# Optimization experiments

Hardware: AMD Instinct MI355X
Metric: run time of the kernel (lower is better)

Reference implementation:

```python
import jax, jax.numpy as jnp
import numpy as np

EPS = 1e-5

def setup_inputs() -> dict:
    key = jax.random.key(0)
    k1, k2, k3 = jax.random.split(key, 3)
    B, D, T = 16, 512, 1024
    K = 8192
    x = jax.random.normal(k1, (B, D, T), dtype=jnp.float32)
    embedding_sum = jax.random.normal(k2, (K, D), dtype=jnp.float32)
    cluster_usage = jax.random.uniform(k3, (K,), dtype=jnp.float32)
    return {"x": x, "embedding_sum": embedding_sum, "cluster_usage": cluster_usage}

def reference(x, embedding_sum, cluster_usage):
    # embedding = embedding_sum / clamp(cluster_usage, eps)  -> [K, D]
    emb = embedding_sum / jnp.clip(cluster_usage, EPS, None)[:, None]
    B, D, T = x.shape
    # encode: [B, D, T] -> [B*T, D]
    xf = jnp.transpose(x, (0, 2, 1)).reshape(B * T, D)
    # squared Euclidean distance (argmin-equivalent to cdist p=2)
    x2 = jnp.sum(xf * xf, axis=1, keepdims=True)          # [N, 1]
    e2 = jnp.sum(emb * emb, axis=1)                        # [K]
    d2 = x2 - 2.0 * (xf @ emb.T) + e2[None, :]             # [N, K]
    codes = jnp.argmin(d2, axis=-1).reshape(B, 1, T)       # [B, 1, T]
    # decode: gather codebook vectors
    quantized = emb[codes[:, 0, :]]                        # [B, T, D]
    quantized = jnp.transpose(quantized, (0, 2, 1))        # [B, D, T]
    return codes, quantized
```

## Files before the change

kernel.cpp:

```cpp
#include <hip/hip_runtime.h>
#include <hip/hip_bf16.h>
#include <cfloat>
#include <stdint.h>

#define EPS 1e-5f
constexpr int Dd = 512, Tt = 1024, Kk = 8192;
constexpr int Nq = 16 * 1024;
constexpr float TAU = 1.5f;

typedef __bf16 bf16x8 __attribute__((ext_vector_type(8)));
typedef float  f32x4  __attribute__((ext_vector_type(4)));
typedef unsigned long long u64;

union Pack8 { __bf16 h[8]; int4 v; };

__device__ __forceinline__ void gld16(const void* g, void* l) {
    __builtin_amdgcn_global_load_lds(
        (const __attribute__((address_space(1))) uint32_t*)g,
        (__attribute__((address_space(3))) uint32_t*)l, 16, 0, 0);
}

__device__ __forceinline__ unsigned monokey(float s) {
    unsigned b = __float_as_uint(s);
    return b ^ ((unsigned)((int)b >> 31) | 0x80000000u);
}
__device__ __forceinline__ float unmono(unsigned u) {
    u = (u & 0x80000000u) ? (u ^ 0x80000000u) : ~u;
    return __uint_as_float(u);
}

__device__ __forceinline__ void merge2u(unsigned& a1, unsigned& a2, unsigned b1, unsigned b2) {
    unsigned c1 = min(a1, b1);
    unsigned c2 = min(max(a1, b1), min(a2, b2));
    a1 = c1; a2 = c2;
}
__device__ __forceinline__ u64 umin64(u64 a, u64 b) { return a < b ? a : b; }
__device__ __forceinline__ u64 umax64(u64 a, u64 b) { return a > b ? a : b; }
__device__ __forceinline__ void merge4q(u64& a1, u64& a2, u64& a3, u64& a4,
                                        u64 b1, u64 b2, u64 b3, u64 b4) {
    u64 c1 = umin64(a1, b1);
    u64 c2 = umin64(umin64(a2, b2), umax64(a1, b1));
    u64 c3 = umin64(umin64(a3, b3), umin64(umax64(a2, b1), umax64(a1, b2)));
    u64 c4 = umin64(umin64(a4, b4), umin64(umax64(a3, b1), umax64(a1, b3)));
    c4 = umin64(c4, umax64(a2, b2));
    a1 = c1; a2 = c2; a3 = c3; a4 = c4;
}
__device__ __forceinline__ u64 shflx64(u64 v, int m) {
    int lo = __shfl_xor((int)(unsigned)v, m, 64);
    int hi = __shfl_xor((int)(v >> 32), m, 64);
    return ((u64)(unsigned)hi << 32) | (unsigned)lo;
}

__global__ __launch_bounds__(256) void split_x_kernel(const float* __restrict__ x,
                                                      ushort* __restrict__ Xh,
                                                      float* __restrict__ Xf,
                                                      int* __restrict__ cnt) {
    if (blockIdx.x == 0 && threadIdx.x < 2) cnt[threadIdx.x] = 0;
    __shared__ float Ls[64][68];
    const int tid = threadIdx.x, bid = blockIdx.x;
    const int b  = bid >> 7;
    const int d0 = ((bid >> 4) & 7) * 64;
    const int t0 = (bid & 15) * 64;
    const float* xb = x + ((size_t)b * Dd + d0) * Tt + t0;
#pragma unroll
    for (int it = 0; it < 4; ++it) {
        int s = it * 256 + tid;
        int d = s >> 4, c = (s & 15) * 4;
        float4 g = *(const float4*)(xb + (size_t)d * Tt + c);
        *(float4*)&Ls[d][c] = g;
    }
    __syncthreads();
    const int t = tid >> 2;
    const int dseg = (tid & 3) * 16;
    Pack8 ph[2];
    float vf[16];
#pragma unroll
    for (int dd = 0; dd < 16; ++dd) {
        float v = Ls[dseg + dd][t];
        vf[dd] = v;
        ph[dd >> 3].h[dd & 7] = (__bf16)v;
    }
    size_t base = ((size_t)(b * Tt + t0 + t)) * Dd + d0 + dseg;
    *(int4*)(Xh + base)     = ph[0].v;
    *(int4*)(Xh + base + 8) = ph[1].v;
#pragma unroll
    for (int g = 0; g < 4; ++g)
        *(float4*)(Xf + base + g * 4) = make_float4(vf[g*4], vf[g*4+1], vf[g*4+2], vf[g*4+3]);
}

__global__ __launch_bounds__(256) void split_e_kernel(const float* __restrict__ es,
                                                      const float* __restrict__ usage,
                                                      ushort* __restrict__ Eh,
                                                      float* __restrict__ embf,
                                                      double* __restrict__ e2d,
                                                      float* __restrict__ e2f) {
    const int wave = threadIdx.x >> 6, lane = threadIdx.x & 63;
    const int k = blockIdx.x * 4 + wave;
    const float uc = fmaxf(usage[k], EPS);
    const float* row = es + (size_t)k * Dd;
    const int d = lane * 8;
    float4 a = *(const float4*)(row + d);
    float4 c = *(const float4*)(row + d + 4);
    float ef[8] = {a.x/uc, a.y/uc, a.z/uc, a.w/uc, c.x/uc, c.y/uc, c.z/uc, c.w/uc};
    Pack8 ph;
    double e2 = 0.0;
#pragma unroll
    for (int j = 0; j < 8; ++j) {
        ph.h[j] = (__bf16)ef[j];
        e2 = fma((double)ef[j], (double)ef[j], e2);
    }
    size_t base = (size_t)k * Dd + d;
    *(int4*)(Eh + base) = ph.v;
    *(float4*)(embf + base)     = make_float4(ef[0], ef[1], ef[2], ef[3]);
    *(float4*)(embf + base + 4) = make_float4(ef[4], ef[5], ef[6], ef[7]);
#pragma unroll
    for (int off = 32; off >= 1; off >>= 1) e2 += __shfl_down(e2, off, 64);
    if (lane == 0) { e2d[k] = e2; e2f[k] = (float)e2; }
}

__device__ __forceinline__ void stageA2(const ushort* __restrict__ Xh, char* buf,
                                        int m0, int d0, int tid, int j0) {
#pragma unroll
    for (int j = 0; j < 2; ++j) {
        int s = (j0 + j) * 512 + tid;
        int row = s >> 3;
        int clog = (s & 7) ^ (row & 7);
        gld16(Xh + (size_t)(m0 + row) * Dd + d0 + clog * 8, buf + s * 16);
    }
}
__device__ __forceinline__ void stageB2(const ushort* __restrict__ Eh, char* buf,
                                        int n0, int d0, int tid, int j0) {
#pragma unroll
    for (int j = 0; j < 2; ++j) {
        int s = (j0 + j) * 512 + tid;
        int row = s >> 3;
        int clog = (s & 7) ^ (row & 7);
        gld16(Eh + (size_t)(n0 + row) * Dd + d0 + clog * 8, buf + 32768 + s * 16);
    }
}

#define SB() __builtin_amdgcn_sched_barrier(0)

__global__ __launch_bounds__(512) void gemm_kernel(const ushort* __restrict__ Xh,
                                                   const ushort* __restrict__ Eh,
                                                   const float* __restrict__ e2f,
                                                   uint2* __restrict__ colres) {
    __shared__ int4 ldsbuf[8192];
    char* lds = (char*)ldsbuf;

    const int tid = threadIdx.x;
    int wg = blockIdx.x;
    int wgid = (wg & 7) * 256 + (wg >> 3);
    int st = wgid >> 5, u = wgid & 31;
    int mb = (st >> 3) * 8 + (u & 7);
    int nb = (st & 7) * 4 + (u >> 3);
    const int m0 = mb * 256, n0 = nb * 256;

    const int wave = tid >> 6, lane = tid & 63;
    const int wm = wave >> 1, wn = wave & 1;
    const int mw = wm * 64, nw = wn * 128;
    const int fm = lane & 15, fq = lane >> 4;
    const int fm7 = fm & 7;
    const int x0 = (fq ^ fm7) * 16;
    const int x1 = ((4 + fq) ^ fm7) * 16;

    f32x4 acc[8][4] = {};

    stageA2(Xh, lds, m0, 0, tid, 0);
    stageA2(Xh, lds, m0, 0, tid, 2);
    stageB2(Eh, lds, n0, 0, tid, 0);
    stageB2(Eh, lds, n0, 0, tid, 2);
    stageA2(Xh, lds + 65536, m0, 64, tid, 0);
    asm volatile("s_waitcnt vmcnt(2)" ::: "memory");
    __builtin_amdgcn_s_barrier();
    SB();

    for (int t = 0; t < 8; ++t) {
        char* bufc = lds + (t & 1) * 65536;
        char* bufn = lds + ((t + 1) & 1) * 65536;
        const char* pA = bufc + (mw + fm) * 128;
        const char* pB = bufc + 32768 + (nw + fm) * 128;
        const int d1 = (t + 1) * 64, d2 = (t + 2) * 64;
        bf16x8 a0[4], a1[4], fr[4];

#pragma unroll
        for (int i = 0; i < 4; ++i) a0[i] = *(const bf16x8*)(pA + i * 2048 + x0);
#pragma unroll
        for (int i = 0; i < 4; ++i) fr[i] = *(const bf16x8*)(pB + i * 2048 + x0);
        SB();
        if (t + 1 < 8) stageA2(Xh, bufn, m0, d1, tid, 2);
        SB();
        __builtin_amdgcn_s_barrier();
        asm volatile("s_waitcnt lgkmcnt(0)" ::: "memory");
        SB();
        __builtin_amdgcn_s_setprio(1);
#pragma unroll
        for (int i = 0; i < 4; ++i)
#pragma unroll
            for (int j = 0; j < 4; ++j)
                acc[i][j] = __builtin_amdgcn_mfma_f32_16x16x32_bf16(fr[i], a0[j], acc[i][j], 0, 0, 0);
        __builtin_amdgcn_s_setprio(0);
        SB();
        __builtin_amdgcn_s_barrier();

#pragma unroll
        for (int i = 0; i < 4; ++i) fr[i] = *(const bf16x8*)(pB + 8192 + i * 2048 + x0);
        SB();
        if (t + 1 < 8) stageB2(Eh, bufn, n0, d1, tid, 0);
        SB();
        __builtin_amdgcn_s_barrier();
        asm volatile("s_waitcnt lgkmcnt(0)" ::: "memory");
        SB();
        __builtin_amdgcn_s_setprio(1);
#pragma unroll
        for (int i = 0; i < 4; ++i)
#pragma unroll
            for (int j = 0; j < 4; ++j)
                acc[i + 4][j] = __builtin_amdgcn_mfma_f32_16x16x32_bf16(fr[i], a0[j], acc[i + 4][j], 0, 0, 0);
        __builtin_amdgcn_s_setprio(0);
        SB();
        __builtin_amdgcn_s_barrier();

#pragma unroll
        for (int i = 0; i < 4; ++i) a1[i] = *(const bf16x8*)(pA + i * 2048 + x1);
#pragma unroll
        for (int i = 0; i < 4; ++i) fr[i] = *(const bf16x8*)(pB + i * 2048 + x1);
        SB();
        if (t + 1 < 8) stageB2(Eh, bufn, n0, d1, tid, 2);
        SB();
        __builtin_amdgcn_s_barrier();
        asm volatile("s_waitcnt lgkmcnt(0)" ::: "memory");
        SB();
        __builtin_amdgcn_s_setprio(1);
#pragma unroll
        for (int i = 0; i < 4; ++i)
#pragma unroll
            for (int j = 0; j < 4; ++j)
                acc[i][j] = __builtin_amdgcn_mfma_f32_16x16x32_bf16(fr[i], a1[j], acc[i][j], 0, 0, 0);
        __builtin_amdgcn_s_setprio(0);
        SB();
        __builtin_amdgcn_s_barrier();

#pragma unroll
        for (int i = 0; i < 4; ++i) fr[i] = *(const bf16x8*)(pB + 8192 + i * 2048 + x1);
        SB();
        if (t + 2 < 8) stageA2(Xh, bufc, m0, d2, tid, 0);
        SB();
        __builtin_amdgcn_s_barrier();
        asm volatile("s_waitcnt lgkmcnt(0)" ::: "memory");
        SB();
        __builtin_amdgcn_s_setprio(1);
#pragma unroll
        for (int i = 0; i < 4; ++i)
#pragma unroll
            for (int j = 0; j < 4; ++j)
                acc[i + 4][j] = __builtin_amdgcn_mfma_f32_16x16x32_bf16(fr[i], a1[j], acc[i + 4][j], 0, 0, 0);
        __builtin_amdgcn_s_setprio(0);
        SB();
        if (t <= 5)      { asm volatile("s_waitcnt vmcnt(2)" ::: "memory"); SB(); }
        else if (t == 6) { asm volatile("s_waitcnt vmcnt(0)" ::: "memory"); SB(); }
        if (t < 7) __builtin_amdgcn_s_barrier();
    }

    float4 e2v[8];
#pragma unroll
    for (int ni = 0; ni < 8; ++ni)
        e2v[ni] = *(const float4*)(e2f + n0 + nw + ni * 16 + fq * 4);

    const int cb = (n0 + nw) >> 7;
#pragma unroll
    for (int mj = 0; mj < 4; ++mj) {
        unsigned s1 = 0xFFFFFFFFu, s2 = 0xFFFFFFFFu;
#pragma unroll
        for (int ni = 0; ni < 8; ++ni) {
            unsigned k0 = (monokey(fmaf(-2.0f, acc[ni][mj][0], e2v[ni].x)) & 0xFFFFFF80u) | (unsigned)(ni * 16 + fq * 4 + 0);
            unsigned k1 = (monokey(fmaf(-2.0f, acc[ni][mj][1], e2v[ni].y)) & 0xFFFFFF80u) | (unsigned)(ni * 16 + fq * 4 + 1);
            unsigned k2 = (monokey(fmaf(-2.0f, acc[ni][mj][2], e2v[ni].z)) & 0xFFFFFF80u) | (unsigned)(ni * 16 + fq * 4 + 2);
            unsigned k3 = (monokey(fmaf(-2.0f, acc[ni][mj][3], e2v[ni].w)) & 0xFFFFFF80u) | (unsigned)(ni * 16 + fq * 4 + 3);
            unsigned lo01 = min(k0, k1), hi01 = max(k0, k1);
            unsigned lo23 = min(k2, k3), hi23 = max(k2, k3);
            unsigned p1 = min(lo01, lo23);
            unsigned p2 = min(max(lo01, lo23), min(hi01, hi23));
            merge2u(s1, s2, p1, p2);
        }
#pragma unroll
        for (int stg = 16; stg <= 32; stg <<= 1) {
            unsigned b1 = __shfl_xor(s1, stg, 64);
            unsigned b2 = __shfl_xor(s2, stg, 64);
            merge2u(s1, s2, b1, b2);
        }
        if (lane < 16)
            colres[(size_t)(m0 + mw + mj * 16 + lane) * 64 + cb] = make_uint2(s1, s2);
    }
}

__global__ __launch_bounds__(256) void merge_kernel(const uint2* __restrict__ colres,
                                                    float* __restrict__ out,
                                                    int* __restrict__ cnt,
                                                    int* __restrict__ queueC,
                                                    int* __restrict__ queueF) {
    const int wave = threadIdx.x >> 6, lane = threadIdx.x & 63;
    const int row = blockIdx.x * 4 + wave;
    uint2 q = colres[(size_t)row * 64 + lane];
    const unsigned nb128 = (unsigned)(lane * 128);
    u64 a1 = ((u64)(q.x & 0xFFFFFF80u) << 32) | (nb128 + (q.x & 127u));
    u64 a2 = ((u64)(q.y & 0xFFFFFF80u) << 32) | (nb128 + (q.y & 127u));
    u64 a3 = ~0ull, a4 = ~0ull;
#pragma unroll
    for (int st = 1; st < 64; st <<= 1)
        merge4q(a1, a2, a3, a4, shflx64(a1, st), shflx64(a2, st), shflx64(a3, st), shflx64(a4, st));
    float v1 = unmono((unsigned)(a1 >> 32));
    u64 coll = __ballot(unmono(q.y) < v1 + TAU);
    if (lane == 0) {
        float v2 = unmono((unsigned)(a2 >> 32));
        float v4 = unmono((unsigned)(a4 >> 32));
        int i1 = (int)(unsigned)a1;
        out[row] = (float)i1;
        if (coll != 0ull || (v4 - v1 < TAU)) {
            int p = atomicAdd(&cnt[1], 1);
            queueF[p] = row;
        } else if (v2 - v1 < TAU) {
            int p = atomicAdd(&cnt[0], 1);
            queueC[p * 5]     = row;
            queueC[p * 5 + 1] = i1;
            queueC[p * 5 + 2] = (int)(unsigned)a2;
            queueC[p * 5 + 3] = (int)(unsigned)a3;
            queueC[p * 5 + 4] = (int)(unsigned)a4;
        }
    }
}

__global__ __launch_bounds__(256) void cand_kernel(const float* __restrict__ Xf,
                                                   const float* __restrict__ embf,
                                                   const double* __restrict__ e2d,
                                                   const int* __restrict__ cnt,
                                                   const int* __restrict__ queueC,
                                                   float* __restrict__ out) {
    const int wv = (blockIdx.x << 2) | (threadIdx.x >> 6);
    const int lane = threadIdx.x & 63;
    const int n = cnt[0];
    for (int p = wv; p < n; p += gridDim.x * 4) {
        int row = queueC[p * 5];
        int ci[4] = {queueC[p*5+1], queueC[p*5+2], queueC[p*5+3], queueC[p*5+4]};
        const float* xr = Xf + (size_t)row * Dd + lane * 8;
        float4 xa = *(const float4*)xr;
        float4 xb = *(const float4*)(xr + 4);
        double s[4] = {0.0, 0.0, 0.0, 0.0};
#pragma unroll
        for (int c = 0; c < 4; ++c) {
            const float* er = embf + (size_t)ci[c] * Dd + lane * 8;
            float4 ea = *(const float4*)er;
            float4 eb = *(const float4*)(er + 4);
            double t = 0.0;
            t = fma((double)xa.x, (double)ea.x, t);
            t = fma((double)xa.y, (double)ea.y, t);
            t = fma((double)xa.z, (double)ea.z, t);
            t = fma((double)xa.w, (double)ea.w, t);
            t = fma((double)xb.x, (double)eb.x, t);
            t = fma((double)xb.y, (double)eb.y, t);
            t = fma((double)xb.z, (double)eb.z, t);
            t = fma((double)xb.w, (double)eb.w, t);
            s[c] = t;
        }
#pragma unroll
        for (int off = 32; off >= 1; off >>= 1) {
#pragma unroll
            for (int c = 0; c < 4; ++c) s[c] += __shfl_down(s[c], off, 64);
        }
        if (lane == 0) {
            double bv = DBL_MAX; int bi = 0x7fffffff;
#pragma unroll
            for (int c = 0; c < 4; ++c) {
                double dv = fma(-2.0, s[c], e2d[ci[c]]);
                if (dv < bv || (dv == bv && ci[c] < bi)) { bv = dv; bi = ci[c]; }
            }
            out[row] = (float)bi;
        }
    }
}

__global__ __launch_bounds__(256) void fscan_kernel(const float* __restrict__ Xf,
                                                    const float* __restrict__ embf,
                                                    const double* __restrict__ e2d,
                                                    const int* __restrict__ cnt,
                                                    const int* __restrict__ queueF,
                                                    double* __restrict__ fbv,
                                                    int* __restrict__ fbi) {
    __shared__ float xs[512];
    __shared__ double sv[256];
    __shared__ int si[256];
    const int tid = threadIdx.x;
    const int ntask = cnt[1] * 16;
    for (int task = blockIdx.x; task < ntask; task += gridDim.x) {
        int qi = task >> 4, ch = task & 15;
        int row = queueF[qi];
        __syncthreads();
        for (int d = tid; d < Dd; d += 256)
            xs[d] = Xf[(size_t)row * Dd + d];
        __syncthreads();
        double bv = DBL_MAX; int bi = 0x7fffffff;
#pragma unroll
        for (int c = 0; c < 2; ++c) {
            int k = ch * 512 + c * 256 + tid;
            const float* er = embf + (size_t)k * Dd;
            double a0 = 0, a1 = 0, a2 = 0, a3 = 0;
            for (int d = 0; d < Dd; d += 4) {
                float4 e = *(const float4*)(er + d);
                float4 xv = *(const float4*)&xs[d];
                a0 = fma((double)e.x, (double)xv.x, a0);
                a1 = fma((double)e.y, (double)xv.y, a1);
                a2 = fma((double)e.z, (double)xv.z, a2);
                a3 = fma((double)e.w, (double)xv.w, a3);
            }
            double s = fma(-2.0, (a0 + a1) + (a2 + a3), e2d[k]);
            if (s < bv || (s == bv && k < bi)) { bv = s; bi = k; }
        }
        sv[tid] = bv; si[tid] = bi;
        __syncthreads();
        for (int off = 128; off > 0; off >>= 1) {
            if (tid < off) {
                if (sv[tid + off] < sv[tid] ||
                    (sv[tid + off] == sv[tid] && si[tid + off] < si[tid])) {
                    sv[tid] = sv[tid + off]; si[tid] = si[tid + off];
                }
            }
            __syncthreads();
        }
        if (tid == 0) { fbv[task] = sv[0]; fbi[task] = si[0]; }
    }
}

__global__ void fmerge_kernel(const int* __restrict__ cnt,
                              const int* __restrict__ queueF,
                              const double* __restrict__ fbv,
                              const int* __restrict__ fbi,
                              float* __restrict__ out) {
    const int nF = cnt[1];
    for (int qi = blockIdx.x * 256 + threadIdx.x; qi < nF; qi += gridDim.x * 256) {
        double bv = DBL_MAX; int bi = 0x7fffffff;
        for (int c = 0; c < 16; ++c) {
            double v = fbv[qi * 16 + c]; int i = fbi[qi * 16 + c];
            if (v < bv || (v == bv && i < bi)) { bv = v; bi = i; }
        }
        out[queueF[qi]] = (float)bi;
    }
}

__global__ __launch_bounds__(256) void gather_kernel(const float* __restrict__ embf,
                                                     float* __restrict__ out) {
    __shared__ int cs[64];
    const int tid = threadIdx.x;
    const int m0 = blockIdx.x * 64;
    const int b = m0 >> 10;
    const int t0 = m0 & (Tt - 1);
    if (tid < 64) cs[tid] = (int)out[m0 + tid];
    __syncthreads();
    const int tq = tid & 63;
    const int dg = tid >> 6;
    const int c = cs[tq];
    const float* row = embf + (size_t)c * Dd;
    float* ob = out + Nq + (size_t)b * Dd * Tt + t0 + tq;
#pragma unroll 4
    for (int d = dg * 128; d < dg * 128 + 128; ++d)
        ob[(size_t)d * Tt] = row[d];
}

extern "C" void kernel_launch(void* const* d_in, const int* in_sizes, int n_in,
                              void* d_out, int out_size, void* d_ws, size_t ws_size,
                              hipStream_t stream) {
    const float* x     = (const float*)d_in[0];
    const float* es    = (const float*)d_in[1];
    const float* usage = (const float*)d_in[2];
    float* out = (float*)d_out;

    char* w = (char*)d_ws;
    ushort* Xh = (ushort*)w;   w += (size_t)Nq * Dd * 2;
    ushort* Eh = (ushort*)w;   w += (size_t)Kk * Dd * 2;
    float*  Xf = (float*)w;    w += (size_t)Nq * Dd * 4;
    float*  embf = (float*)w;  w += (size_t)Kk * Dd * 4;
    double* e2d = (double*)w;  w += (size_t)Kk * 8;
    float*  e2f = (float*)w;   w += (size_t)Kk * 4;
    uint2* colres = (uint2*)w; w += (size_t)Nq * 64 * 8;
    int* cnt = (int*)w;        w += 256;
    int* queueC = (int*)w;     w += (size_t)Nq * 5 * 4;
    int* queueF = (int*)w;     w += (size_t)Nq * 4;
    double* fbv = (double*)Xh;
    int*    fbi = (int*)((char*)Xh + 4 * 1024 * 1024);

    split_x_kernel<<<2048, 256, 0, stream>>>(x, Xh, Xf, cnt);
    split_e_kernel<<<Kk / 4, 256, 0, stream>>>(es, usage, Eh, embf, e2d, e2f);
    gemm_kernel<<<2048, 512, 0, stream>>>(Xh, Eh, e2f, colres);
    merge_kernel<<<Nq / 4, 256, 0, stream>>>(colres, out, cnt, queueC, queueF);
    cand_kernel<<<256, 256, 0, stream>>>(Xf, embf, e2d, cnt, queueC, out);
    fscan_kernel<<<256, 256, 0, stream>>>(Xf, embf, e2d, cnt, queueF, fbv, fbi);
    fmerge_kernel<<<64, 256, 0, stream>>>(cnt, queueF, fbv, fbi, out);
    gather_kernel<<<Nq / 64, 256, 0, stream>>>(embf, out);
}
```

Measured before the change: 371.6 us.

## Make GEMM persistent over eight N tiles with cross-tile software pipelining

The distance GEMM now launches 256 workgroups instead of 2048. Each keeps one 256-row M tile and loops over eight N tiles (64 K-steps in total), writing the per-tile top-2 epilogue every eighth step and resetting the accumulators. LDS fragment loads for the next phase are issued before the current MFMAs and use partial lgkmcnt waits instead of full drains, with fewer barriers per phase. This removes workgroup launch and prologue/epilogue bubbles and keeps the pipeline full across tiles. The cost is more live registers and a grid that is exactly one wave of 256 workgroups, so any load imbalance or occupancy loss is exposed.

After: 536.7 us. +44.4%, slower.

```diff
diff --git a/kernel.cpp b/kernel.cpp
--- a/kernel.cpp
+++ b/kernel.cpp
@@ -149,12 +149,10 @@
     char* lds = (char*)ldsbuf;
 
     const int tid = threadIdx.x;
-    int wg = blockIdx.x;
-    int wgid = (wg & 7) * 256 + (wg >> 3);
-    int st = wgid >> 5, u = wgid & 31;
-    int mb = (st >> 3) * 8 + (u & 7);
-    int nb = (st & 7) * 4 + (u >> 3);
-    const int m0 = mb * 256, n0 = nb * 256;
+    const int wg = blockIdx.x;
+    const int xcd = wg & 7, idx = wg >> 3;
+    const int m0 = (xcd * 8 + (idx & 7)) * 256;
+    const int nbase = (idx >> 3) * 256;
 
     const int wave = tid >> 6, lane = tid & 63;
     const int wm = wave >> 1, wn = wave & 1;
@@ -163,134 +161,154 @@
     const int fm7 = fm & 7;
     const int x0 = (fq ^ fm7) * 16;
     const int x1 = ((4 + fq) ^ fm7) * 16;
+    const int pao = (mw + fm) * 128;
+    const int pbo = 32768 + (nw + fm) * 128;
 
     f32x4 acc[8][4] = {};
+    bf16x8 a0[4], a1[4], bl0[4], bh0[4], bl1[4], bh1[4];
 
     stageA2(Xh, lds, m0, 0, tid, 0);
     stageA2(Xh, lds, m0, 0, tid, 2);
-    stageB2(Eh, lds, n0, 0, tid, 0);
-    stageB2(Eh, lds, n0, 0, tid, 2);
+    stageB2(Eh, lds, nbase, 0, tid, 0);
+    stageB2(Eh, lds, nbase, 0, tid, 2);
     stageA2(Xh, lds + 65536, m0, 64, tid, 0);
     asm volatile("s_waitcnt vmcnt(2)" ::: "memory");
     __builtin_amdgcn_s_barrier();
     SB();
-
-    for (int t = 0; t < 8; ++t) {
-        char* bufc = lds + (t & 1) * 65536;
-        char* bufn = lds + ((t + 1) & 1) * 65536;
-        const char* pA = bufc + (mw + fm) * 128;
-        const char* pB = bufc + 32768 + (nw + fm) * 128;
-        const int d1 = (t + 1) * 64, d2 = (t + 2) * 64;
-        bf16x8 a0[4], a1[4], fr[4];
-
-#pragma unroll
-        for (int i = 0; i < 4; ++i) a0[i] = *(const bf16x8*)(pA + i * 2048 + x0);
-#pragma unroll
-        for (int i = 0; i < 4; ++i) fr[i] = *(const bf16x8*)(pB + i * 2048 + x0);
-        SB();
-        if (t + 1 < 8) stageA2(Xh, bufn, m0, d1, tid, 2);
+#pragma unroll
+    for (int i = 0; i < 4; ++i) a0[i]  = *(const bf16x8*)(lds + pao + i * 2048 + x0);
+#pragma unroll
+    for (int i = 0; i < 4; ++i) bl0[i] = *(const bf16x8*)(lds + pbo + i * 2048 + x0);
+    SB();
+
+    for (int v = 0; v < 64; ++v) {
+        char* bufc = lds + (v & 1) * 65536;
+        char* bufn = lds + ((v + 1) & 1) * 65536;
+        const char* pA = bufc + pao;
+        const char* pB = bufc + pbo;
+        const int vn = v + 1, vn2 = v + 2;
+        const int d1 = (vn & 7) * 64, d2 = (vn2 & 7) * 64;
+        const int n0n = (vn >> 3) * 1024 + nbase;
+
+#pragma unroll
+        for (int i = 0; i < 4; ++i) bh0[i] = *(const bf16x8*)(pB + 8192 + i * 2048 + x0);
+        SB();
+        if (vn < 64) stageA2(Xh, bufn, m0, d1, tid, 2);
+        SB();
+        asm volatile("s_waitcnt lgkmcnt(4)" ::: "memory");
+        SB();
+        __builtin_amdgcn_s_setprio(1);
+#pragma unroll
+        for (int i = 0; i < 4; ++i)
+#pragma unroll
+            for (int j = 0; j < 4; ++j)
+                acc[i][j] = __builtin_amdgcn_mfma_f32_16x16x32_bf16(bl0[i], a0[j], acc[i][j], 0, 0, 0);
+        __builtin_amdgcn_s_setprio(0);
         SB();
         __builtin_amdgcn_s_barrier();
+
+#pragma unroll
+        for (int i = 0; i < 4; ++i) a1[i]  = *(const bf16x8*)(pA + i * 2048 + x1);
+#pragma unroll
+        for (int i = 0; i < 4; ++i) bl1[i] = *(const bf16x8*)(pB + i * 2048 + x1);
+        SB();
+        if (vn < 64) stageB2(Eh, bufn, n0n, d1, tid, 0);
+        SB();
+        asm volatile("s_waitcnt lgkmcnt(8)" ::: "memory");
+        SB();
+        __builtin_amdgcn_s_setprio(1);
+#pragma unroll
+        for (int i = 0; i < 4; ++i)
+#pragma unroll
+            for (int j = 0; j < 4; ++j)
+                acc[i + 4][j] = __builtin_amdgcn_mfma_f32_16x16x32_bf16(bh0[i], a0[j], acc[i + 4][j], 0, 0, 0);
+        __builtin_amdgcn_s_setprio(0);
+        SB();
+        __builtin_amdgcn_s_barrier();
+
+#pragma unroll
+        for (int i = 0; i < 4; ++i) bh1[i] = *(const bf16x8*)(pB + 8192 + i * 2048 + x1);
+        SB();
+        if (vn < 64) stageB2(Eh, bufn, n0n, d1, tid, 2);
+        SB();
+        asm volatile("s_waitcnt lgkmcnt(4)" ::: "memory");
+        SB();
+        __builtin_amdgcn_s_setprio(1);
+#pragma unroll
+        for (int i = 0; i < 4; ++i)
+#pragma unroll
+            for (int j = 0; j < 4; ++j)
+                acc[i][j] = __builtin_amdgcn_mfma_f32_16x16x32_bf16(bl1[i], a1[j], acc[i][j], 0, 0, 0);
+        __builtin_amdgcn_s_setprio(0);
+        SB();
+        __builtin_amdgcn_s_barrier();
+
         asm volatile("s_waitcnt lgkmcnt(0)" ::: "memory");
         SB();
+        __builtin_amdgcn_s_barrier();
+        if (vn2 < 64) stageA2(Xh, bufc, m0, d2, tid, 0);
+        SB();
         __builtin_amdgcn_s_setprio(1);
 #pragma unroll
         for (int i = 0; i < 4; ++i)
 #pragma unroll
             for (int j = 0; j < 4; ++j)
-                acc[i][j] = __builtin_amdgcn_mfma_f32_16x16x32_bf16(fr[i], a0[j], acc[i][j], 0, 0, 0);
+                acc[i + 4][j] = __builtin_amdgcn_mfma_f32_16x16x32_bf16(bh1[i], a1[j], acc[i + 4][j], 0, 0, 0);
         __builtin_amdgcn_s_setprio(0);
         SB();
-        __builtin_amdgcn_s_barrier();
-
-#pragma unroll
-        for (int i = 0; i < 4; ++i) fr[i] = *(const bf16x8*)(pB + 8192 + i * 2048 + x0);
-        SB();
-        if (t + 1 < 8) stageB2(Eh, bufn, n0, d1, tid, 0);
-        SB();
-        __builtin_amdgcn_s_barrier();
-        asm volatile("s_waitcnt lgkmcnt(0)" ::: "memory");
-        SB();
-        __builtin_amdgcn_s_setprio(1);
-#pragma unroll
-        for (int i = 0; i < 4; ++i)
-#pragma unroll
-            for (int j = 0; j < 4; ++j)
-                acc[i + 4][j] = __builtin_amdgcn_mfma_f32_16x16x32_bf16(fr[i], a0[j], acc[i + 4][j], 0, 0, 0);
-        __builtin_amdgcn_s_setprio(0);
-        SB();
-        __builtin_amdgcn_s_barrier();
-
-#pragma unroll
-        for (int i = 0; i < 4; ++i) a1[i] = *(const bf16x8*)(pA + i * 2048 + x1);
-#pragma unroll
-        for (int i = 0; i < 4; ++i) fr[i] = *(const bf16x8*)(pB + i * 2048 + x1);
-        SB();
-        if (t + 1 < 8) stageB2(Eh, bufn, n0, d1, tid, 2);
-        SB();
-        __builtin_amdgcn_s_barrier();
-        asm volatile("s_waitcnt lgkmcnt(0)" ::: "memory");
-        SB();
-        __builtin_amdgcn_s_setprio(1);
-#pragma unroll
-        for (int i = 0; i < 4; ++i)
-#pragma unroll
-            for (int j = 0; j < 4; ++j)
-                acc[i][j] = __builtin_amdgcn_mfma_f32_16x16x32_bf16(fr[i], a1[j], acc[i][j], 0, 0, 0);
-        __builtin_amdgcn_s_setprio(0);
-        SB();
-        __builtin_amdgcn_s_barrier();
-
-#pragma unroll
-        for (int i = 0; i < 4; ++i) fr[i] = *(const bf16x8*)(pB + 8192 + i * 2048 + x1);
-        SB();
-        if (t + 2 < 8) stageA2(Xh, bufc, m0, d2, tid, 0);
-        SB();
-        __builtin_amdgcn_s_barrier();
-        asm volatile("s_waitcnt lgkmcnt(0)" ::: "memory");
-        SB();
-        __builtin_amdgcn_s_setprio(1);
-#pragma unroll
-        for (int i = 0; i < 4; ++i)
-#pragma unroll
-            for (int j = 0; j < 4; ++j)
-                acc[i + 4][j] = __builtin_amdgcn_mfma_f32_16x16x32_bf16(fr[i], a1[j], acc[i + 4][j], 0, 0, 0);
-        __builtin_amdgcn_s_setprio(0);
-        SB();
-        if (t <= 5)      { asm volatile("s_waitcnt vmcnt(2)" ::: "memory"); SB(); }
-        else if (t == 6) { asm volatile("s_waitcnt vmcnt(0)" ::: "memory"); SB(); }
-        if (t < 7) __builtin_amdgcn_s_barrier();
-    }
-
-    float4 e2v[8];
-#pragma unroll
-    for (int ni = 0; ni < 8; ++ni)
-        e2v[ni] = *(const float4*)(e2f + n0 + nw + ni * 16 + fq * 4);
-
-    const int cb = (n0 + nw) >> 7;
-#pragma unroll
-    for (int mj = 0; mj < 4; ++mj) {
-        unsigned s1 = 0xFFFFFFFFu, s2 = 0xFFFFFFFFu;
-#pragma unroll
-        for (int ni = 0; ni < 8; ++ni) {
-            unsigned k0 = (monokey(fmaf(-2.0f, acc[ni][mj][0], e2v[ni].x)) & 0xFFFFFF80u) | (unsigned)(ni * 16 + fq * 4 + 0);
-            unsigned k1 = (monokey(fmaf(-2.0f, acc[ni][mj][1], e2v[ni].y)) & 0xFFFFFF80u) | (unsigned)(ni * 16 + fq * 4 + 1);
-            unsigned k2 = (monokey(fmaf(-2.0f, acc[ni][mj][2], e2v[ni].z)) & 0xFFFFFF80u) | (unsigned)(ni * 16 + fq * 4 + 2);
-            unsigned k3 = (monokey(fmaf(-2.0f, acc[ni][mj][3], e2v[ni].w)) & 0xFFFFFF80u) | (unsigned)(ni * 16 + fq * 4 + 3);
-            unsigned lo01 = min(k0, k1), hi01 = max(k0, k1);
-            unsigned lo23 = min(k2, k3), hi23 = max(k2, k3);
-            unsigned p1 = min(lo01, lo23);
-            unsigned p2 = min(max(lo01, lo23), min(hi01, hi23));
-            merge2u(s1, s2, p1, p2);
-        }
-#pragma unroll
-        for (int stg = 16; stg <= 32; stg <<= 1) {
-            unsigned b1 = __shfl_xor(s1, stg, 64);
-            unsigned b2 = __shfl_xor(s2, stg, 64);
-            merge2u(s1, s2, b1, b2);
-        }
-        if (lane < 16)
-            colres[(size_t)(m0 + mw + mj * 16 + lane) * 64 + cb] = make_uint2(s1, s2);
+
+        if ((v & 7) == 7) {
+            const int n0 = (v >> 3) * 1024 + nbase;
+            float4 e2v[8];
+#pragma unroll
+            for (int ni = 0; ni < 8; ++ni)
+                e2v[ni] = *(const float4*)(e2f + n0 + nw + ni * 16 + fq * 4);
+            const int cb = (n0 + nw) >> 7;
+#pragma unroll
+            for (int mj = 0; mj < 4; ++mj) {
+                unsigned s1 = 0xFFFFFFFFu, s2 = 0xFFFFFFFFu;
+#pragma unroll
+                for (int ni = 0; ni < 8; ++ni) {
+                    unsigned k0 = (monokey(fmaf(-2.0f, acc[ni][mj][0], e2v[ni].x)) & 0xFFFFFF80u) | (unsigned)(ni * 16 + fq * 4 + 0);
+                    unsigned k1 = (monokey(fmaf(-2.0f, acc[ni][mj][1], e2v[ni].y)) & 0xFFFFFF80u) | (unsigned)(ni * 16 + fq * 4 + 1);
+                    unsigned k2 = (monokey(fmaf(-2.0f, acc[ni][mj][2], e2v[ni].z)) & 0xFFFFFF80u) | (unsigned)(ni * 16 + fq * 4 + 2);
+                    unsigned k3 = (monokey(fmaf(-2.0f, acc[ni][mj][3], e2v[ni].w)) & 0xFFFFFF80u) | (unsigned)(ni * 16 + fq * 4 + 3);
+                    unsigned lo01 = min(k0, k1), hi01 = max(k0, k1);
+                    unsigned lo23 = min(k2, k3), hi23 = max(k2, k3);
+                    unsigned p1 = min(lo01, lo23);
+                    unsigned p2 = min(max(lo01, lo23), min(hi01, hi23));
+                    merge2u(s1, s2, p1, p2);
+                }
+#pragma unroll
+                for (int stg = 16; stg <= 32; stg <<= 1) {
+                    unsigned b1 = __shfl_xor(s1, stg, 64);
+                    unsigned b2 = __shfl_xor(s2, stg, 64);
+                    merge2u(s1, s2, b1, b2);
+                }
+                if (lane < 16)
+                    colres[(size_t)(m0 + mw + mj * 16 + lane) * 64 + cb] = make_uint2(s1, s2);
+            }
+#pragma unroll
+            for (int i = 0; i < 8; ++i)
+#pragma unroll
+                for (int j = 0; j < 4; ++j)
+                    acc[i][j] = (f32x4){0.f, 0.f, 0.f, 0.f};
+        }
+
+        if (v < 63) {
+            if (v < 62) { asm volatile("s_waitcnt vmcnt(2)" ::: "memory"); }
+            else        { asm volatile("s_waitcnt vmcnt(0)" ::: "memory"); }
+            SB();
+            __builtin_amdgcn_s_barrier();
+            SB();
+            const char* pAn = bufn + pao;
+            const char* pBn = bufn + pbo;
+#pragma unroll
+            for (int i = 0; i < 4; ++i) a0[i]  = *(const bf16x8*)(pAn + i * 2048 + x0);
+#pragma unroll
+            for (int i = 0; i < 4; ++i) bl0[i] = *(const bf16x8*)(pBn + i * 2048 + x0);
+            SB();
+        }
     }
 }
 
@@ -489,7 +507,7 @@
 
     split_x_kernel<<<2048, 256, 0, stream>>>(x, Xh, Xf, cnt);
     split_e_kernel<<<Kk / 4, 256, 0, stream>>>(es, usage, Eh, embf, e2d, e2f);
-    gemm_kernel<<<2048, 512, 0, stream>>>(Xh, Eh, e2f, colres);
+    gemm_kernel<<<256, 512, 0, stream>>>(Xh, Eh, e2f, colres);
     merge_kernel<<<Nq / 4, 256, 0, stream>>>(colres, out, cnt, queueC, queueF);
     cand_kernel<<<256, 256, 0, stream>>>(Xf, embf, e2d, cnt, queueC, out);
     fscan_kernel<<<256, 256, 0, stream>>>(Xf, embf, e2d, cnt, queueF, fbv, fbi);
```
